# Kernel optimization log

Hardware: AMD Instinct MI355X
Metric: run time of the kernel (lower is better)

Reference implementation:

```python
import jax, jax.numpy as jnp
import numpy as np

B, S, D = 8, 2048, 512

def setup_inputs() -> dict:
    key = jax.random.key(0)
    ks = jax.random.split(key, 9)
    scale = 1.0 / np.sqrt(D)
    return {
        "x": jax.random.normal(ks[0], (B, S, D), dtype=jnp.float32),
        "attention_mask": jax.random.uniform(ks[1], (B, S), dtype=jnp.float32),
        "Wq": jax.random.normal(ks[2], (D, D), dtype=jnp.float32) * scale,
        "bq": jax.random.normal(ks[3], (D,), dtype=jnp.float32) * 0.01,
        "Wk": jax.random.normal(ks[4], (D, D), dtype=jnp.float32) * scale,
        "bk": jax.random.normal(ks[5], (D,), dtype=jnp.float32) * 0.01,
        "Wv": jax.random.normal(ks[6], (D, D), dtype=jnp.float32) * scale,
        "bv": jax.random.normal(ks[7], (D,), dtype=jnp.float32) * 0.01,
    }

def reference(x, attention_mask, Wq, bq, Wk, bk, Wv, bv):
    # Single-head self-attention, full O(S^2) scores as in the original.
    q = jnp.einsum('bsd,df->bsf', x, Wq) + bq  # [B,S,D]
    k = jnp.einsum('bsd,df->bsf', x, Wk) + bk
    v = jnp.einsum('bsd,df->bsf', x, Wv) + bv
    scores = jnp.einsum('bqd,bkd->bqk', q, k) / jnp.sqrt(jnp.float32(D))  # [B,S,S]
    attn = jax.nn.softmax(scores, axis=2)
    weighted = jnp.einsum('bqk,bkd->bqd', attn, v)  # [B,S,D]
    # mask applied multiplicatively to the output, per original code
    return weighted * attention_mask[:, :, None]
```

## Files before the change

### kernel.cpp

```cpp
#include <hip/hip_runtime.h>
#include <math.h>
#include <stdint.h>


typedef _Float16 f16x8 __attribute__((ext_vector_type(8)));
typedef _Float16 f16x4 __attribute__((ext_vector_type(4)));
typedef float f32x4 __attribute__((ext_vector_type(4)));

__device__ __forceinline__ void async16(const _Float16* g, _Float16* l) {
    __builtin_amdgcn_global_load_lds(
        (const __attribute__((address_space(1))) unsigned int*)(uintptr_t)g,
        (__attribute__((address_space(3))) unsigned int*)(unsigned int)(uintptr_t)l,
        16, 0, 0);
}

__device__ __forceinline__ void mfma_gemm_core64(
    const _Float16* __restrict__ A, int lda,
    const _Float16* __restrict__ B, int ldb,
    int K, int row0, int col0,
    _Float16* As, _Float16* Bs, f32x4 acc[4][4])
{
    const int tid  = threadIdx.x;
    const int lane = tid & 63;
    const int wave = tid >> 6;
    const int wm   = wave >> 1, wn = wave & 1;

    const int rc  = lane >> 3;
    const int swz = ((lane & 7) ^ rc) * 8;

    const _Float16* gA[4]; const _Float16* gB[4];
    _Float16* lA[4]; _Float16* lB[4];
#pragma unroll
    for (int i = 0; i < 4; i++) {
        int c = wave * 4 + i;
        gA[i] = A + (size_t)(row0 + 8 * c + rc) * lda + swz;
        gB[i] = B + (size_t)(col0 + 8 * c + rc) * ldb + swz;
        lA[i] = As + c * 512;
        lB[i] = Bs + c * 512;
    }

    const int fr = lane & 15;
    const int q  = lane >> 4;
    const int fx = fr & 7;

    for (int k0 = 0; k0 < K; k0 += 64) {
        __syncthreads();
#pragma unroll
        for (int i = 0; i < 4; i++) {
            async16(gA[i] + k0, lA[i]);
            async16(gB[i] + k0, lB[i]);
        }
        __syncthreads();
#pragma unroll
        for (int step = 0; step < 2; step++) {
            f16x8 af[4], bf[4];
#pragma unroll
            for (int t = 0; t < 4; t++) {
                int ra = wm * 64 + t * 16 + fr;
                int rb = wn * 64 + t * 16 + fr;
                int kc = ((step * 4 + q) ^ fx) * 8;
                af[t] = *(const f16x8*)&As[ra * 64 + kc];
                bf[t] = *(const f16x8*)&Bs[rb * 64 + kc];
            }
#pragma unroll
            for (int tm = 0; tm < 4; tm++)
#pragma unroll
                for (int tn = 0; tn < 4; tn++)
                    acc[tm][tn] = __builtin_amdgcn_mfma_f32_16x16x32_f16(
                        af[tm], bf[tn], acc[tm][tn], 0, 0, 0);
        }
    }
}

__global__ __launch_bounds__(256) void convert_x(
    const float* __restrict__ x, _Float16* __restrict__ Xh)
{
    int i = (blockIdx.x * 256 + threadIdx.x) * 4;
    float4 v = *(const float4*)(x + i);
    f16x4 h;
    h.x = (_Float16)v.x; h.y = (_Float16)v.y;
    h.z = (_Float16)v.z; h.w = (_Float16)v.w;
    *(f16x4*)&Xh[i] = h;
}

__global__ __launch_bounds__(256) void transpose_w(
    const float* __restrict__ Wq, const float* __restrict__ Wk,
    const float* __restrict__ Wv,
    _Float16* __restrict__ WqT, _Float16* __restrict__ WkT,
    _Float16* __restrict__ WvT)
{
    const float* W; _Float16* Wt;
    if (blockIdx.z == 0)      { W = Wq; Wt = WqT; }
    else if (blockIdx.z == 1) { W = Wk; Wt = WkT; }
    else                      { W = Wv; Wt = WvT; }
    int idx = blockIdx.x * 256 + threadIdx.x;
    int n = idx >> 9, k = idx & 511;
    Wt[idx] = (_Float16)W[k * 512 + n];
}

__global__ __launch_bounds__(256) void proj_mfma(
    const _Float16* __restrict__ Xh,
    const _Float16* __restrict__ WqT, const float* __restrict__ bq,
    const _Float16* __restrict__ WkT, const float* __restrict__ bk,
    const _Float16* __restrict__ WvT, const float* __restrict__ bv,
    _Float16* __restrict__ Qh, _Float16* __restrict__ Kh,
    _Float16* __restrict__ Vt)
{
    __shared__ __align__(16) _Float16 smem[2 * 128 * 64];
    _Float16* As = smem;
    _Float16* Bs = smem + 128 * 64;

    const int z = blockIdx.z;
    f32x4 acc[4][4];
#pragma unroll
    for (int i = 0; i < 4; i++)
#pragma unroll
        for (int j = 0; j < 4; j++) acc[i][j] = (f32x4){0.f, 0.f, 0.f, 0.f};

    const int lane = threadIdx.x & 63, wave = threadIdx.x >> 6;
    const int wm = wave >> 1, wn = wave & 1;
    const int er = (lane >> 4) * 4, ec = lane & 15;

    if (z < 2) {
        const _Float16* Wt = (z == 0) ? WqT : WkT;
        const float* bias  = (z == 0) ? bq : bk;
        _Float16* P        = (z == 0) ? Qh : Kh;
        const int row0 = blockIdx.y * 128, col0 = blockIdx.x * 128;
        mfma_gemm_core64(Xh, 512, Wt, 512, 512, row0, col0, As, Bs, acc);
#pragma unroll
        for (int tm = 0; tm < 4; tm++)
#pragma unroll
            for (int tn = 0; tn < 4; tn++) {
                int col = col0 + wn * 64 + tn * 16 + ec;
                float bb = bias[col];
#pragma unroll
                for (int r = 0; r < 4; r++) {
                    int row = row0 + wm * 64 + tm * 16 + er + r;
                    P[(size_t)row * 512 + col] = (_Float16)(acc[tm][tn][r] + bb);
                }
            }
    } else {
        const int row0 = blockIdx.x * 128;
        const int col0 = blockIdx.y * 128;
        mfma_gemm_core64(WvT, 512, Xh, 512, 512, row0, col0, As, Bs, acc);
#pragma unroll
        for (int tm = 0; tm < 4; tm++)
#pragma unroll
            for (int tn = 0; tn < 4; tn++) {
                int col = col0 + wn * 64 + tn * 16 + ec;
                size_t obase = (size_t)(col >> 11) * (512 * 2048) + (col & 2047);
#pragma unroll
                for (int r = 0; r < 4; r++) {
                    int row = row0 + wm * 64 + tm * 16 + er + r;
                    Vt[obase + (size_t)row * 2048] = (_Float16)(acc[tm][tn][r] + bv[row]);
                }
            }
    }
}

__global__ __launch_bounds__(256) void zero_l(float* __restrict__ l)
{
    l[blockIdx.x * 256 + threadIdx.x] = 0.f;
}

__global__ __launch_bounds__(256) void scores_mfma(
    const _Float16* __restrict__ Qh, const _Float16* __restrict__ Kh,
    _Float16* __restrict__ Sh, float* __restrict__ lsum)
{
    __shared__ __align__(16) _Float16 smem[2 * 128 * 64];
    _Float16* As = smem;
    _Float16* Bs = smem + 128 * 64;
    const int bid = blockIdx.x;
    const int b   = bid & 7;
    const int rem = bid >> 3;
    const int col0 = (rem & 15) * 128;
    const int row0 = (rem >> 4) * 128;

    const _Float16* A = Qh + (size_t)b * 2048 * 512;
    const _Float16* B = Kh + (size_t)b * 2048 * 512;
    _Float16* S = Sh + (size_t)b * 2048 * 2048;
    float* lb = lsum + b * 2048;

    f32x4 acc[4][4];
#pragma unroll
    for (int i = 0; i < 4; i++)
#pragma unroll
        for (int j = 0; j < 4; j++) acc[i][j] = (f32x4){0.f, 0.f, 0.f, 0.f};

    mfma_gemm_core64(A, 512, B, 512, 512, row0, col0, As, Bs, acc);

    const float scale = 0.04419417382415922f;
    const int lane = threadIdx.x & 63, wave = threadIdx.x >> 6;
    const int wm = wave >> 1, wn = wave & 1;
    const int er = (lane >> 4) * 4, ec = lane & 15;

    float rsum[4][4];
#pragma unroll
    for (int tm = 0; tm < 4; tm++)
#pragma unroll
        for (int r = 0; r < 4; r++) rsum[tm][r] = 0.f;

#pragma unroll
    for (int tm = 0; tm < 4; tm++)
#pragma unroll
        for (int tn = 0; tn < 4; tn++) {
            int col = col0 + wn * 64 + tn * 16 + ec;
#pragma unroll
            for (int r = 0; r < 4; r++) {
                int row = row0 + wm * 64 + tm * 16 + er + r;
                float e = __expf(acc[tm][tn][r] * scale);
                rsum[tm][r] += e;
                S[(size_t)row * 2048 + col] = (_Float16)e;
            }
        }
#pragma unroll
    for (int m = 1; m < 16; m <<= 1)
#pragma unroll
        for (int tm = 0; tm < 4; tm++)
#pragma unroll
            for (int r = 0; r < 4; r++)
                rsum[tm][r] += __shfl_xor(rsum[tm][r], m, 64);
    if (ec == 0) {
#pragma unroll
        for (int tm = 0; tm < 4; tm++)
#pragma unroll
            for (int r = 0; r < 4; r++) {
                int row = row0 + wm * 64 + tm * 16 + er + r;
                atomicAdd(&lb[row], rsum[tm][r]);
            }
    }
}

__global__ __launch_bounds__(256) void av_mfma(
    const _Float16* __restrict__ Sh, const _Float16* __restrict__ Vt,
    const float* __restrict__ mask, const float* __restrict__ lsum,
    float* __restrict__ out)
{
    __shared__ __align__(16) _Float16 smem[2 * 128 * 64];
    _Float16* As = smem;
    _Float16* Bs = smem + 128 * 64;
    const int bid = blockIdx.x;
    const int b   = bid & 7;
    const int rem = bid >> 3;
    const int col0 = (rem & 3) * 128;
    const int row0 = (rem >> 2) * 128;

    const _Float16* A = Sh + (size_t)b * 2048 * 2048;
    const _Float16* B = Vt + (size_t)b * 512 * 2048;
    float* O = out + (size_t)b * 2048 * 512;
    const float* mk = mask + (size_t)b * 2048;
    const float* lb = lsum + b * 2048;

    f32x4 acc[4][4];
#pragma unroll
    for (int i = 0; i < 4; i++)
#pragma unroll
        for (int j = 0; j < 4; j++) acc[i][j] = (f32x4){0.f, 0.f, 0.f, 0.f};

    mfma_gemm_core64(A, 2048, B, 2048, 2048, row0, col0, As, Bs, acc);

    const int lane = threadIdx.x & 63, wave = threadIdx.x >> 6;
    const int wm = wave >> 1, wn = wave & 1;
    const int er = (lane >> 4) * 4, ec = lane & 15;
#pragma unroll
    for (int tm = 0; tm < 4; tm++)
#pragma unroll
        for (int r = 0; r < 4; r++) {
            int row = row0 + wm * 64 + tm * 16 + er + r;
            float s = mk[row] / lb[row];
#pragma unroll
            for (int tn = 0; tn < 4; tn++) {
                int col = col0 + wn * 64 + tn * 16 + ec;
                O[(size_t)row * 512 + col] = acc[tm][tn][r] * s;
            }
        }
}

extern "C" void kernel_launch(void* const* d_in, const int* in_sizes, int n_in,
                              void* d_out, int out_size, void* d_ws, size_t ws_size,
                              hipStream_t stream) {
    const float* x    = (const float*)d_in[0];
    const float* mask = (const float*)d_in[1];
    const float* Wq   = (const float*)d_in[2];
    const float* bq   = (const float*)d_in[3];
    const float* Wk   = (const float*)d_in[4];
    const float* bk   = (const float*)d_in[5];
    const float* Wv   = (const float*)d_in[6];
    const float* bv   = (const float*)d_in[7];
    float* out = (float*)d_out;

    const size_t BSD = (size_t)8 * 2048 * 512;
    _Float16* base = (_Float16*)d_ws;
    _Float16* Qh  = base;
    _Float16* Kh  = Qh + BSD;
    _Float16* Vt  = Kh + BSD;
    _Float16* WqT = Vt + BSD;
    _Float16* WkT = WqT + 512 * 512;
    _Float16* WvT = WkT + 512 * 512;
    _Float16* Xh  = WvT + 512 * 512;
    _Float16* Sh  = Xh;
    float*    lsum = (float*)WqT;

    dim3 blk(256);
    convert_x<<<dim3(BSD / 4 / 256), blk, 0, stream>>>(x, Xh);
    transpose_w<<<dim3(512 * 512 / 256, 1, 3), blk, 0, stream>>>(
        Wq, Wk, Wv, WqT, WkT, WvT);
    proj_mfma<<<dim3(4, 128, 3), blk, 0, stream>>>(
        Xh, WqT, bq, WkT, bk, WvT, bv, Qh, Kh, Vt);
    zero_l<<<dim3(16384 / 256), blk, 0, stream>>>(lsum);
    scores_mfma<<<dim3(2048), blk, 0, stream>>>(Qh, Kh, Sh, lsum);
    av_mfma<<<dim3(512), blk, 0, stream>>>(Sh, Vt, mask, lsum, out);
}
```

Measured before the change: 256.5 us.

## Fuse scores, softmax and AV into a single flash-style attention kernel

Replaces the separate scores kernel, which wrote a full fp16 exp-score matrix to global memory, and the AV GEMM kernel with one fused kernel. Each 32-row query block loops over key tiles, computes exp scores in registers, stages them in LDS and multiplies them straight into V. The 1/sqrt(D) scale is folded into the Q projection epilogue, and row sums are reduced inside the block instead of by atomics, which removes the zeroing kernel. This avoids the large S matrix round trip to memory. In exchange, Q is reloaded for every key tile, each block does a lot of synchronisation, and there is no max subtraction, the same as before.

Result: slower. 430.7 us (+67.9%).

```diff
diff --git a/kernel.cpp b/kernel.cpp
--- a/kernel.cpp
+++ b/kernel.cpp
@@ -125,6 +125,7 @@
         const _Float16* Wt = (z == 0) ? WqT : WkT;
         const float* bias  = (z == 0) ? bq : bk;
         _Float16* P        = (z == 0) ? Qh : Kh;
+        const float sc     = (z == 0) ? 0.04419417382415922f : 1.0f;
         const int row0 = blockIdx.y * 128, col0 = blockIdx.x * 128;
         mfma_gemm_core64(Xh, 512, Wt, 512, 512, row0, col0, As, Bs, acc);
 #pragma unroll
@@ -136,7 +137,7 @@
 #pragma unroll
                 for (int r = 0; r < 4; r++) {
                     int row = row0 + wm * 64 + tm * 16 + er + r;
-                    P[(size_t)row * 512 + col] = (_Float16)(acc[tm][tn][r] + bb);
+                    P[(size_t)row * 512 + col] = (_Float16)((acc[tm][tn][r] + bb) * sc);
                 }
             }
     } else {
@@ -158,120 +159,158 @@
     }
 }
 
-__global__ __launch_bounds__(256) void zero_l(float* __restrict__ l)
-{
-    l[blockIdx.x * 256 + threadIdx.x] = 0.f;
-}
-
-__global__ __launch_bounds__(256) void scores_mfma(
+__global__ __launch_bounds__(256) void attn_fused(
     const _Float16* __restrict__ Qh, const _Float16* __restrict__ Kh,
-    _Float16* __restrict__ Sh, float* __restrict__ lsum)
-{
-    __shared__ __align__(16) _Float16 smem[2 * 128 * 64];
-    _Float16* As = smem;
-    _Float16* Bs = smem + 128 * 64;
-    const int bid = blockIdx.x;
-    const int b   = bid & 7;
-    const int rem = bid >> 3;
-    const int col0 = (rem & 15) * 128;
-    const int row0 = (rem >> 4) * 128;
-
-    const _Float16* A = Qh + (size_t)b * 2048 * 512;
-    const _Float16* B = Kh + (size_t)b * 2048 * 512;
-    _Float16* S = Sh + (size_t)b * 2048 * 2048;
-    float* lb = lsum + b * 2048;
-
-    f32x4 acc[4][4];
-#pragma unroll
-    for (int i = 0; i < 4; i++)
-#pragma unroll
-        for (int j = 0; j < 4; j++) acc[i][j] = (f32x4){0.f, 0.f, 0.f, 0.f};
-
-    mfma_gemm_core64(A, 512, B, 512, 512, row0, col0, As, Bs, acc);
-
-    const float scale = 0.04419417382415922f;
-    const int lane = threadIdx.x & 63, wave = threadIdx.x >> 6;
-    const int wm = wave >> 1, wn = wave & 1;
-    const int er = (lane >> 4) * 4, ec = lane & 15;
-
-    float rsum[4][4];
-#pragma unroll
-    for (int tm = 0; tm < 4; tm++)
-#pragma unroll
-        for (int r = 0; r < 4; r++) rsum[tm][r] = 0.f;
-
-#pragma unroll
-    for (int tm = 0; tm < 4; tm++)
-#pragma unroll
-        for (int tn = 0; tn < 4; tn++) {
-            int col = col0 + wn * 64 + tn * 16 + ec;
-#pragma unroll
-            for (int r = 0; r < 4; r++) {
-                int row = row0 + wm * 64 + tm * 16 + er + r;
-                float e = __expf(acc[tm][tn][r] * scale);
-                rsum[tm][r] += e;
-                S[(size_t)row * 2048 + col] = (_Float16)e;
-            }
-        }
+    const _Float16* __restrict__ Vt, const float* __restrict__ mask,
+    float* __restrict__ out)
+{
+    __shared__ __align__(16) _Float16 stage[20480];
+    __shared__ __align__(16) _Float16 Pb[4096];
+    __shared__ float lred[4][32];
+    _Float16* Qs0 = stage;
+    _Float16* Qs1 = stage + 2048;
+    _Float16* Ks0 = stage + 4096;
+    _Float16* Ks1 = stage + 12288;
+    _Float16* Vs  = stage;
+
+    const int tid = threadIdx.x, lane = tid & 63, wv = tid >> 6;
+    const int b  = blockIdx.x & 7;
+    const int rt = blockIdx.x >> 3;
+    const int brow0 = rt * 32;
+
+    const _Float16* Qb = Qh + (size_t)b * 2048 * 512;
+    const _Float16* Kb = Kh + (size_t)b * 2048 * 512;
+    const _Float16* Vb = Vt + (size_t)b * 512 * 2048;
+
+    const int rc  = lane >> 3;
+    const int swz = ((lane & 7) ^ rc) * 8;
+    const int fr  = lane & 15;
+    const int kq  = lane >> 4;
+    const int fx  = fr & 7;
+
+    f32x4 oacc[2][8];
+#pragma unroll
+    for (int tm = 0; tm < 2; tm++)
+#pragma unroll
+        for (int tn = 0; tn < 8; tn++) oacc[tm][tn] = (f32x4){0.f, 0.f, 0.f, 0.f};
+    float rs[2][4] = {};
+
+    const _Float16* gQ = Qb + (size_t)(brow0 + 8 * wv + rc) * 512 + swz;
+
+    for (int j = 0; j < 16; j++) {
+        f32x4 sacc[2][2];
+#pragma unroll
+        for (int tm = 0; tm < 2; tm++)
+#pragma unroll
+            for (int tn = 0; tn < 2; tn++) sacc[tm][tn] = (f32x4){0.f, 0.f, 0.f, 0.f};
+
+        for (int k0 = 0; k0 < 512; k0 += 128) {
+            __syncthreads();
+            async16(gQ + k0,      Qs0 + wv * 512);
+            async16(gQ + k0 + 64, Qs1 + wv * 512);
+#pragma unroll
+            for (int i = 0; i < 4; i++) {
+                int c = wv * 4 + i;
+                const _Float16* src =
+                    Kb + (size_t)(j * 128 + 8 * c + rc) * 512 + k0 + swz;
+                async16(src,      Ks0 + c * 512);
+                async16(src + 64, Ks1 + c * 512);
+            }
+            __syncthreads();
+#pragma unroll
+            for (int step = 0; step < 4; step++) {
+                const _Float16* Qs = (step < 2) ? Qs0 : Qs1;
+                const _Float16* Ks = (step < 2) ? Ks0 : Ks1;
+                int kc = (((step & 1) * 4 + kq) ^ fx) * 8;
+                f16x8 aq[2], bk[2];
+#pragma unroll
+                for (int t = 0; t < 2; t++) {
+                    aq[t] = *(const f16x8*)&Qs[(t * 16 + fr) * 64 + kc];
+                    bk[t] = *(const f16x8*)&Ks[(wv * 32 + t * 16 + fr) * 64 + kc];
+                }
+#pragma unroll
+                for (int tm = 0; tm < 2; tm++)
+#pragma unroll
+                    for (int tn = 0; tn < 2; tn++)
+                        sacc[tm][tn] = __builtin_amdgcn_mfma_f32_16x16x32_f16(
+                            aq[tm], bk[tn], sacc[tm][tn], 0, 0, 0);
+            }
+        }
+
+#pragma unroll
+        for (int tm = 0; tm < 2; tm++)
+#pragma unroll
+            for (int tn = 0; tn < 2; tn++) {
+                int col = wv * 32 + tn * 16 + fr;
+#pragma unroll
+                for (int r = 0; r < 4; r++) {
+                    int row = tm * 16 + kq * 4 + r;
+                    float e = __expf(sacc[tm][tn][r]);
+                    rs[tm][r] += e;
+                    int phys = (col >> 3) ^ (row & 7);
+                    Pb[row * 128 + phys * 8 + (col & 7)] = (_Float16)e;
+                }
+            }
+
+        for (int ks = 0; ks < 4; ks++) {
+            __syncthreads();
+#pragma unroll
+            for (int i = 0; i < 8; i++) {
+                int d = i * 64 + lane;
+                const _Float16* src =
+                    Vb + (size_t)d * 2048 + j * 128 + ks * 32 + wv * 8;
+                async16(src, Vs + (wv * 512 + i * 64) * 8);
+            }
+            __syncthreads();
+            f16x8 ap[2];
+#pragma unroll
+            for (int tm = 0; tm < 2; tm++) {
+                int row = tm * 16 + fr;
+                int phys = (ks * 4 + kq) ^ fx;
+                ap[tm] = *(const f16x8*)&Pb[row * 128 + phys * 8];
+            }
+#pragma unroll
+            for (int tn = 0; tn < 8; tn++) {
+                int d = wv * 128 + tn * 16 + fr;
+                f16x8 bv8 = *(const f16x8*)&Vs[(kq * 512 + d) * 8];
+#pragma unroll
+                for (int tm = 0; tm < 2; tm++)
+                    oacc[tm][tn] = __builtin_amdgcn_mfma_f32_16x16x32_f16(
+                        ap[tm], bv8, oacc[tm][tn], 0, 0, 0);
+            }
+        }
+    }
+
 #pragma unroll
     for (int m = 1; m < 16; m <<= 1)
 #pragma unroll
-        for (int tm = 0; tm < 4; tm++)
+        for (int tm = 0; tm < 2; tm++)
 #pragma unroll
             for (int r = 0; r < 4; r++)
-                rsum[tm][r] += __shfl_xor(rsum[tm][r], m, 64);
-    if (ec == 0) {
-#pragma unroll
-        for (int tm = 0; tm < 4; tm++)
-#pragma unroll
-            for (int r = 0; r < 4; r++) {
-                int row = row0 + wm * 64 + tm * 16 + er + r;
-                atomicAdd(&lb[row], rsum[tm][r]);
-            }
-    }
-}
-
-__global__ __launch_bounds__(256) void av_mfma(
-    const _Float16* __restrict__ Sh, const _Float16* __restrict__ Vt,
-    const float* __restrict__ mask, const float* __restrict__ lsum,
-    float* __restrict__ out)
-{
-    __shared__ __align__(16) _Float16 smem[2 * 128 * 64];
-    _Float16* As = smem;
-    _Float16* Bs = smem + 128 * 64;
-    const int bid = blockIdx.x;
-    const int b   = bid & 7;
-    const int rem = bid >> 3;
-    const int col0 = (rem & 3) * 128;
-    const int row0 = (rem >> 2) * 128;
-
-    const _Float16* A = Sh + (size_t)b * 2048 * 2048;
-    const _Float16* B = Vt + (size_t)b * 512 * 2048;
+                rs[tm][r] += __shfl_xor(rs[tm][r], m, 64);
+    if (fr == 0) {
+#pragma unroll
+        for (int tm = 0; tm < 2; tm++)
+#pragma unroll
+            for (int r = 0; r < 4; r++)
+                lred[wv][tm * 16 + kq * 4 + r] = rs[tm][r];
+    }
+    __syncthreads();
+
+    const float* mk = mask + (size_t)b * 2048;
     float* O = out + (size_t)b * 2048 * 512;
-    const float* mk = mask + (size_t)b * 2048;
-    const float* lb = lsum + b * 2048;
-
-    f32x4 acc[4][4];
-#pragma unroll
-    for (int i = 0; i < 4; i++)
-#pragma unroll
-        for (int j = 0; j < 4; j++) acc[i][j] = (f32x4){0.f, 0.f, 0.f, 0.f};
-
-    mfma_gemm_core64(A, 2048, B, 2048, 2048, row0, col0, As, Bs, acc);
-
-    const int lane = threadIdx.x & 63, wave = threadIdx.x >> 6;
-    const int wm = wave >> 1, wn = wave & 1;
-    const int er = (lane >> 4) * 4, ec = lane & 15;
-#pragma unroll
-    for (int tm = 0; tm < 4; tm++)
+#pragma unroll
+    for (int tm = 0; tm < 2; tm++)
 #pragma unroll
         for (int r = 0; r < 4; r++) {
-            int row = row0 + wm * 64 + tm * 16 + er + r;
-            float s = mk[row] / lb[row];
-#pragma unroll
-            for (int tn = 0; tn < 4; tn++) {
-                int col = col0 + wn * 64 + tn * 16 + ec;
-                O[(size_t)row * 512 + col] = acc[tm][tn][r] * s;
+            int lrow = tm * 16 + kq * 4 + r;
+            int grow = brow0 + lrow;
+            float l = lred[0][lrow] + lred[1][lrow] + lred[2][lrow] + lred[3][lrow];
+            float s = mk[grow] / l;
+#pragma unroll
+            for (int tn = 0; tn < 8; tn++) {
+                int col = wv * 128 + tn * 16 + fr;
+                O[(size_t)grow * 512 + col] = oacc[tm][tn][r] * s;
             }
         }
 }
@@ -298,8 +337,6 @@
     _Float16* WkT = WqT + 512 * 512;
     _Float16* WvT = WkT + 512 * 512;
     _Float16* Xh  = WvT + 512 * 512;
-    _Float16* Sh  = Xh;
-    float*    lsum = (float*)WqT;
 
     dim3 blk(256);
     convert_x<<<dim3(BSD / 4 / 256), blk, 0, stream>>>(x, Xh);
@@ -307,7 +344,5 @@
         Wq, Wk, Wv, WqT, WkT, WvT);
     proj_mfma<<<dim3(4, 128, 3), blk, 0, stream>>>(
         Xh, WqT, bq, WkT, bk, WvT, bv, Qh, Kh, Vt);
-    zero_l<<<dim3(16384 / 256), blk, 0, stream>>>(lsum);
-    scores_mfma<<<dim3(2048), blk, 0, stream>>>(Qh, Kh, Sh, lsum);
-    av_mfma<<<dim3(512), blk, 0, stream>>>(Sh, Vt, mask, lsum, out);
-}
+    attn_fused<<<dim3(512), blk, 0, stream>>>(Qh, Kh, Vt, mask, out);
+}
```
